# Kernel tuning notes

Hardware: AMD Instinct MI355X
Metric: run time of the kernel (lower is better)

The kernel has to match this reference:

```python
import jax, jax.numpy as jnp
import numpy as np


def setup_inputs() -> dict:
    key = jax.random.key(0)
    B, T, H, L = 64, 512, 768, 25
    ks = jax.random.split(key, 6)
    encoder_logits = jax.random.normal(ks[0], (B, T, H), dtype=jnp.float32)
    attention_mask = jnp.ones((B, T), dtype=jnp.int32)  # torchcrf requires mask[:,0]==1
    labels = jax.random.randint(ks[1], (B, T), 0, L, dtype=jnp.int32)
    W_em = jax.random.normal(ks[2], (H, L), dtype=jnp.float32) * 0.02
    b_em = jnp.zeros((L,), dtype=jnp.float32)
    # CRF.reset_parameters draws Uniform(-0.1, 0.1)
    trans = jax.random.uniform(ks[3], (L, L), minval=-0.1, maxval=0.1, dtype=jnp.float32)
    start_t = jax.random.uniform(ks[4], (L,), minval=-0.1, maxval=0.1, dtype=jnp.float32)
    end_t = jax.random.uniform(ks[5], (L,), minval=-0.1, maxval=0.1, dtype=jnp.float32)
    return {
        "encoder_logits": encoder_logits,
        "attention_mask": attention_mask,
        "labels": labels,
        "W_em": W_em,
        "b_em": b_em,
        "trans": trans,
        "start_t": start_t,
        "end_t": end_t,
    }


def _crf_llh(emissions, tags, mask, start_t, end_t, trans):
    # emissions: [B,T,L], tags: [B,T] int, mask: [B,T] {0,1}
    maskf = mask.astype(emissions.dtype)
    # ---- numerator: score of the gold path ----
    em_tag = jnp.take_along_axis(emissions, tags[..., None], axis=2)[..., 0]  # [B,T]
    num = start_t[tags[:, 0]] + em_tag[:, 0]
    tr = trans[tags[:, :-1], tags[:, 1:]]  # [B,T-1]
    num = num + jnp.sum((tr + em_tag[:, 1:]) * maskf[:, 1:], axis=1)
    last_idx = jnp.sum(mask, axis=1).astype(jnp.int32) - 1  # [B]
    last_tags = jnp.take_along_axis(tags, last_idx[:, None], axis=1)[:, 0]
    num = num + end_t[last_tags]
    # ---- denominator: log partition via forward algorithm (scan over time) ----
    alpha0 = start_t[None, :] + emissions[:, 0]  # [B,L]
    em_t = jnp.moveaxis(emissions[:, 1:], 1, 0)  # [T-1,B,L]
    m_t = jnp.moveaxis(maskf[:, 1:], 1, 0)       # [T-1,B]

    def step(alpha, xs):
        em, m = xs
        # broadcast [B,L,1] + [L,L] + [B,1,L] -> logsumexp over source tag
        nxt = jax.nn.logsumexp(alpha[:, :, None] + trans[None, :, :] + em[:, None, :], axis=1)
        return jnp.where(m[:, None] > 0, nxt, alpha), None

    alphaT, _ = jax.lax.scan(step, alpha0, (em_t, m_t))
    denom = jax.nn.logsumexp(alphaT + end_t[None, :], axis=1)  # [B]
    return num - denom


def reference(encoder_logits, attention_mask, labels, W_em, b_em, trans, start_t, end_t):
    # dropout layers are identity in eval mode
    emissions = jnp.einsum("bth,hl->btl", encoder_logits, W_em) + b_em
    llh = _crf_llh(emissions, labels, attention_mask, start_t, end_t, trans)
    # torchcrf reduction='mean' averages log-likelihood over batch; module returns -llh
    return -jnp.mean(llh)
```

## Files before the change

### kernel.cpp

```cpp
#include <hip/hip_runtime.h>
#include <hip/hip_bf16.h>

#define NB 64
#define NT 512
#define NH 768
#define NL 25
#define EST 28
#define SEGS 32
#define SEGLEN 16

typedef __attribute__((ext_vector_type(8))) short bf16x8;
typedef __attribute__((ext_vector_type(4))) float f32x4;
typedef __attribute__((ext_vector_type(16))) float f32x16;

__device__ __forceinline__ float readlane_f(float v, int k) {
  return __int_as_float(__builtin_amdgcn_readlane(__float_as_int(v), k));
}

__device__ __forceinline__ short f2bf(float x) {
  uint32_t u = __float_as_uint(x);
  uint32_t r = (u + 0x7fffu + ((u >> 16) & 1u)) >> 16;
  return (short)r;
}

__device__ __forceinline__ int cvt_pk_bf16(float lo, float hi) {
  int r;
  asm("v_cvt_pk_bf16_f32 %0, %1, %2" : "=v"(r) : "v"(lo), "v"(hi));
  return r;
}

__global__ __launch_bounds__(256) void emis_mfma_kernel(
    const float* __restrict__ X, const int* __restrict__ mask,
    const float* __restrict__ W, const float* __restrict__ bias,
    float* __restrict__ em) {
  __shared__ bf16x8 Bf[2][24][64];
  const int tid = threadIdx.x;

#pragma unroll
  for (int it = 0; it < 12; ++it) {
    int idx = tid + it * 256;
    int nt = idx / (24 * 64);
    int rem = idx - nt * (24 * 64);
    int ks = rem >> 6;
    int sl = rem & 63;
    int col = (sl & 15) + nt * 16;
    int kb = ks * 32 + (sl >> 4) * 8;
    bf16x8 f;
#pragma unroll
    for (int j = 0; j < 8; ++j) {
      float v = (col < NL) ? W[(kb + j) * NL + col] : 0.f;
      f[j] = f2bf(v);
    }
    Bf[nt][ks][sl] = f;
  }
  __syncthreads();

  const int wave = tid >> 6;
  const int lane = tid & 63;
  const int rowTile = blockIdx.x * 64 + wave * 16;
  const int row = rowTile + (lane & 15);
  const int koff = (lane >> 4) * 8;
  const float4* __restrict__ xr = (const float4*)(X + (size_t)row * NH + koff);

  f32x4 acc0 = {0.f, 0.f, 0.f, 0.f};
  f32x4 acc1 = {0.f, 0.f, 0.f, 0.f};
#pragma unroll 4
  for (int ks = 0; ks < 24; ++ks) {
    float4 xa = xr[ks * 8];
    float4 xb = xr[ks * 8 + 1];
    bf16x8 a;
    a[0] = f2bf(xa.x); a[1] = f2bf(xa.y); a[2] = f2bf(xa.z); a[3] = f2bf(xa.w);
    a[4] = f2bf(xb.x); a[5] = f2bf(xb.y); a[6] = f2bf(xb.z); a[7] = f2bf(xb.w);
    bf16x8 b0 = Bf[0][ks][lane];
    bf16x8 b1 = Bf[1][ks][lane];
    acc0 = __builtin_amdgcn_mfma_f32_16x16x32_bf16(a, b0, acc0, 0, 0, 0);
    acc1 = __builtin_amdgcn_mfma_f32_16x16x32_bf16(a, b1, acc1, 0, 0, 0);
  }

  const int cg = lane & 15;
  const int rbase = rowTile + (lane >> 4) * 4;
  float b0v = bias[cg];
  float b1v = (cg < 9) ? bias[16 + cg] : 0.f;
#pragma unroll
  for (int r = 0; r < 4; ++r) {
    int ro = rbase + r;
    float* er = em + (size_t)ro * EST;
    er[cg] = acc0[r] + b0v;
    if (cg < 9)       er[16 + cg] = acc1[r] + b1v;
    else if (cg == 9) er[25] = (float)mask[ro];
  }
}

__global__ __launch_bounds__(64) void crf_seg_kernel(
    const float* __restrict__ em, const float* __restrict__ trans,
    float* __restrict__ Dg, float* __restrict__ Dc) {
  const int b = blockIdx.x / SEGS;
  const int s = blockIdx.x % SEGS;
  const int lane = threadIdx.x;
  const int l = lane & 31;
  const int half = lane >> 5;
  const float* __restrict__ emb = em + (size_t)b * NT * EST;

  float Et0[8], Et1[8];
#pragma unroll
  for (int j = 0; j < 8; ++j) {
    int k0 = 8 * half + j;
    int k1 = 16 + 8 * half + j;
    Et0[j] = (l < NL) ? __expf(trans[k0 * NL + l]) : 0.f;
    Et1[j] = (l < NL && k1 < NL) ? __expf(trans[k1 * NL + l]) : 0.f;
  }

  f32x16 acc;
#pragma unroll
  for (int r = 0; r < 16; ++r) {
    int row = (r & 3) + 8 * (r >> 2) + 4 * half;
    acc[r] = (row == l && l < NL) ? 1.f : 0.f;
  }

  union Frag { int i[4]; bf16x8 v; };
  Frag B0, B1;
#pragma unroll
  for (int m = 0; m < 4; ++m) {
    int ka = 8 * half + 2 * m, kb = ka + 1;
    B0.i[m] = cvt_pk_bf16((ka == l && l < NL) ? 1.f : 0.f,
                          (kb == l && l < NL) ? 1.f : 0.f);
    int kc = 16 + 8 * half + 2 * m, kd = kc + 1;
    B1.i[m] = cvt_pk_bf16((kc == l && l < NL) ? 1.f : 0.f,
                          (kd == l && l < NL) ? 1.f : 0.f);
  }

  const int ts = 1 + s * SEGLEN;
  const int te = (ts + SEGLEN < NT) ? ts + SEGLEN : NT;
  const int c2 = (l < NL) ? l : NL;

  float c = 0.f, sc = 1.f, ei_ln2 = 0.f;

  float p0 = emb[ts * EST + c2];
  int i1 = ts + 1 < te ? ts + 1 : te - 1;
  int i2 = ts + 2 < te ? ts + 2 : te - 1;
  int i3 = ts + 3 < te ? ts + 3 : te - 1;
  float p1 = emb[i1 * EST + c2];
  float p2 = emb[i2 * EST + c2];
  float p3 = emb[i3 * EST + c2];

  for (int t = ts; t < te; ++t) {
    float emv = p0; p0 = p1; p1 = p2; p2 = p3;
    int tp = t + 4 < te ? t + 4 : te - 1;
    p3 = emb[tp * EST + c2];

    float mv = readlane_f(emv, 25);
    if (mv > 0.f) {
      float g = __expf(emv) * sc;
      c += ei_ln2;
      sc = 1.f; ei_ln2 = 0.f;

      Frag A0, A1;
#pragma unroll
      for (int m = 0; m < 4; ++m) {
        A0.i[m] = cvt_pk_bf16(Et0[2 * m] * g, Et0[2 * m + 1] * g);
        A1.i[m] = cvt_pk_bf16(Et1[2 * m] * g, Et1[2 * m + 1] * g);
      }
      f32x16 z;
#pragma unroll
      for (int r = 0; r < 16; ++r) z[r] = 0.f;
      z = __builtin_amdgcn_mfma_f32_32x32x16_bf16(A0.v, B0.v, z, 0, 0, 0);
      acc = __builtin_amdgcn_mfma_f32_32x32x16_bf16(A1.v, B1.v, z, 0, 0, 0);

      if ((t & 7) == 7) {
        float a0s = readlane_f(acc[0], 0);
        int eb = (__float_as_int(a0s) >> 23) & 255;
        int ei = (eb == 0) ? 0 : eb - 127;
        sc = __int_as_float((127 - ei) << 23);
        ei_ln2 = (float)ei * 0.6931471805599453f;
      }

      int u0 = cvt_pk_bf16(acc[0], acc[1]);
      int u1 = cvt_pk_bf16(acc[2], acc[3]);
      int w0 = cvt_pk_bf16(acc[4], acc[5]);
      int w1 = cvt_pk_bf16(acc[6], acc[7]);
      asm volatile("v_permlane32_swap_b32 %0, %1" : "+v"(u0), "+v"(w0));
      asm volatile("v_permlane32_swap_b32 %0, %1" : "+v"(u1), "+v"(w1));
      B0.i[0] = u0; B0.i[1] = u1; B0.i[2] = w0; B0.i[3] = w1;
      int v0 = cvt_pk_bf16(acc[8], acc[9]);
      int v1 = cvt_pk_bf16(acc[10], acc[11]);
      int x0 = cvt_pk_bf16(acc[12], acc[13]);
      int x1 = cvt_pk_bf16(acc[14], acc[15]);
      asm volatile("v_permlane32_swap_b32 %0, %1" : "+v"(v0), "+v"(x0));
      asm volatile("v_permlane32_swap_b32 %0, %1" : "+v"(v1), "+v"(x1));
      B1.i[0] = v0; B1.i[1] = v1; B1.i[2] = x0; B1.i[3] = x1;
    }
  }

  float* dst = Dg + (size_t)(b * SEGS + s) * 32 * 32;
#pragma unroll
  for (int r = 0; r < 16; ++r) {
    int row = (r & 3) + 8 * (r >> 2) + 4 * half;
    dst[row * 32 + l] = acc[r];
  }
  if (lane == 0) Dc[b * SEGS + s] = c;
}

__global__ __launch_bounds__(64) void crf_merge_kernel(
    const float* __restrict__ em, const int* __restrict__ labels,
    const int* __restrict__ mask, const float* __restrict__ trans,
    const float* __restrict__ start_t, const float* __restrict__ end_t,
    const float* __restrict__ Dg, const float* __restrict__ Dc,
    float* __restrict__ out) {
  const int b = blockIdx.x;
  const int lane = threadIdx.x;
  const float* __restrict__ emb = em + (size_t)b * NT * EST;
  const int* __restrict__ lb = labels + b * NT;
  const int* __restrict__ mk = mask + b * NT;

  float np = 0.f;
  int ms = 0;
#pragma unroll
  for (int i = 0; i < 8; ++i) {
    int t = lane + i * 64;
    int tag = lb[t];
    int m = mk[t];
    float emt = emb[t * EST + tag];
    ms += m;
    if (t == 0) {
      np += start_t[tag] + emt;
    } else {
      int tagp = lb[t - 1];
      np += (trans[tagp * NL + tag] + emt) * (float)m;
    }
  }
#pragma unroll
  for (int off = 32; off > 0; off >>= 1) {
    np += __shfl_down(np, off, 64);
    ms += __shfl_down(ms, off, 64);
  }
  float num = 0.f;
  if (lane == 0) num = np + end_t[lb[ms - 1]];

  const int l = lane & 31;
  float a = (lane < NL) ? __expf(start_t[lane] + emb[lane]) : 0.f;
  float c = 0.f;
  for (int s = 0; s < SEGS; ++s) {
    const float* Drow = Dg + ((size_t)(b * SEGS + s) * 32 + l) * 32;
    float a0 = 0.f, a1 = 0.f, a2 = 0.f, a3 = 0.f;
#pragma unroll
    for (int i = 0; i < NL; i += 4) {
      a0 = fmaf(Drow[i], readlane_f(a, i), a0);
      if (i + 1 < NL) a1 = fmaf(Drow[i + 1], readlane_f(a, i + 1), a1);
      if (i + 2 < NL) a2 = fmaf(Drow[i + 2], readlane_f(a, i + 2), a2);
      if (i + 3 < NL) a3 = fmaf(Drow[i + 3], readlane_f(a, i + 3), a3);
    }
    float an = (a0 + a1) + (a2 + a3);
    c += Dc[b * SEGS + s];
    float s0 = readlane_f(an, 0);
    int eb = (__float_as_int(s0) >> 23) & 255;
    int ei = (eb == 0) ? 0 : eb - 127;
    a = an * __int_as_float((127 - ei) << 23);
    c += (float)ei * 0.6931471805599453f;
  }

  float v = (lane < NL) ? a * __expf(end_t[lane]) : 0.f;
#pragma unroll
  for (int off = 32; off > 0; off >>= 1) v += __shfl_down(v, off, 64);
  if (lane == 0) {
    float denom = c + __logf(v);
    atomicAdd(out, (denom - num) * (1.0f / (float)NB));
  }
}

__global__ __launch_bounds__(64) void crf_kernel(
    const float* __restrict__ em, const int* __restrict__ labels,
    const int* __restrict__ mask, const float* __restrict__ trans,
    const float* __restrict__ start_t, const float* __restrict__ end_t,
    float* __restrict__ out) {
  const int b = blockIdx.x;
  const int lane = threadIdx.x;
  const int l = lane < NL ? lane : NL - 1;
  const float* __restrict__ emb = em + (size_t)b * NT * EST;
  const int* __restrict__ lb = labels + b * NT;
  const int* __restrict__ mk = mask + b * NT;

  float np = 0.f;
  int ms = 0;
#pragma unroll
  for (int i = 0; i < 8; ++i) {
    int t = lane + i * 64;
    int tag = lb[t];
    int m = mk[t];
    float emt = emb[t * EST + tag];
    ms += m;
    if (t == 0) np += start_t[tag] + emt;
    else {
      int tagp = lb[t - 1];
      np += (trans[tagp * NL + tag] + emt) * (float)m;
    }
  }
#pragma unroll
  for (int off = 32; off > 0; off >>= 1) {
    np += __shfl_down(np, off, 64);
    ms += __shfl_down(ms, off, 64);
  }
  float num = 0.f;
  if (lane == 0) num = np + end_t[lb[ms - 1]];

  float Ecol[NL];
#pragma unroll
  for (int k = 0; k < NL; ++k) Ecol[k] = __expf(trans[k * NL + l]);

  float A = __expf(start_t[l] + emb[l]);
  float c = 0.f, sc = 1.f, ei_ln2 = 0.f;
  const int j = lane < NL ? lane : NL;

  float p1 = emb[1 * EST + j];
  float p2 = emb[2 * EST + j];
  float p3 = emb[3 * EST + j];
  float p4 = emb[4 * EST + j];

  for (int t = 1; t < NT; ++t) {
    float emv = p1;
    p1 = p2; p2 = p3; p3 = p4;
    int tp = t + 4; tp = tp < NT ? tp : NT - 1;
    p4 = emb[tp * EST + j];
    float e_em = __expf(emv);
    float Pv0 = 0.f, Pv1 = 0.f, Pv2 = 0.f, Pv3 = 0.f;
#pragma unroll
    for (int k = 0; k < NL; k += 4) {
      Pv0 = fmaf(readlane_f(A, k), Ecol[k], Pv0);
      if (k + 1 < NL) Pv1 = fmaf(readlane_f(A, k + 1), Ecol[k + 1], Pv1);
      if (k + 2 < NL) Pv2 = fmaf(readlane_f(A, k + 2), Ecol[k + 2], Pv2);
      if (k + 3 < NL) Pv3 = fmaf(readlane_f(A, k + 3), Ecol[k + 3], Pv3);
    }
    float g = ((Pv0 + Pv1) + (Pv2 + Pv3)) * e_em;
    float mfv = readlane_f(emv, 25);
    float An = (mfv > 0.f) ? g : A;
    A = An * sc;
    c += ei_ln2;
    float a0 = readlane_f(A, 0);
    int eb = (__float_as_int(a0) >> 23) & 255;
    int ei = (eb == 0) ? 0 : (eb - 127);
    sc = __int_as_float((127 - ei) << 23);
    ei_ln2 = (float)ei * 0.6931471805599453f;
  }

  float v = (lane < NL) ? A * __expf(end_t[l]) : 0.f;
#pragma unroll
  for (int off = 32; off > 0; off >>= 1) v += __shfl_down(v, off, 64);
  if (lane == 0) {
    float denom = c + __logf(v);
    atomicAdd(out, (denom - num) * (1.0f / (float)NB));
  }
}

extern "C" void kernel_launch(void* const* d_in, const int* in_sizes, int n_in,
                              void* d_out, int out_size, void* d_ws, size_t ws_size,
                              hipStream_t stream) {
  const float* X       = (const float*)d_in[0];
  const int*   mask    = (const int*)d_in[1];
  const int*   labels  = (const int*)d_in[2];
  const float* W       = (const float*)d_in[3];
  const float* bias    = (const float*)d_in[4];
  const float* trans   = (const float*)d_in[5];
  const float* start_t = (const float*)d_in[6];
  const float* end_t   = (const float*)d_in[7];
  float* out = (float*)d_out;

  float* em = (float*)d_ws;
  float* Dg = (float*)((char*)d_ws + (4u << 20));
  float* Dc = (float*)((char*)d_ws + (4u << 20) + (8u << 20));

  hipMemsetAsync(out, 0, sizeof(float), stream);
  emis_mfma_kernel<<<512, 256, 0, stream>>>(X, mask, W, bias, em);
  if (ws_size >= (13u << 20)) {
    crf_seg_kernel<<<NB * SEGS, 64, 0, stream>>>(em, trans, Dg, Dc);
    crf_merge_kernel<<<NB, 64, 0, stream>>>(em, labels, mask, trans, start_t,
                                            end_t, Dg, Dc, out);
  } else {
    crf_kernel<<<NB, 64, 0, stream>>>(em, labels, mask, trans, start_t, end_t, out);
  }
}
```

Measured before the change: 198.7 us.

## Pre-pack W into bf16 MFMA fragments and compute emissions without LDS

Adds a small kernel that converts W once per call into bf16 MFMA B-fragment layout in workspace. The emission GEMM becomes a one-wave-per-16-row kernel that reads X and the packed W straight from global memory, with no LDS staging or per-block W conversion. The aim is to remove the repeated per-block conversion of W and the LDS traffic, and to raise parallelism to 2048 small blocks. The cost is an extra kernel launch and redundant global/L2 reads of the packed W by every wave. The workspace layout shifts and the fast path now requires a larger workspace.

```diff
diff --git a/kernel.cpp b/kernel.cpp
--- a/kernel.cpp
+++ b/kernel.cpp
@@ -13,6 +13,8 @@
 typedef __attribute__((ext_vector_type(4))) float f32x4;
 typedef __attribute__((ext_vector_type(16))) float f32x16;
 
+union Frag { int i[4]; bf16x8 v; };
+
 __device__ __forceinline__ float readlane_f(float v, int k) {
   return __int_as_float(__builtin_amdgcn_readlane(__float_as_int(v), k));
 }
@@ -27,6 +29,68 @@
   int r;
   asm("v_cvt_pk_bf16_f32 %0, %1, %2" : "=v"(r) : "v"(lo), "v"(hi));
   return r;
+}
+
+__global__ __launch_bounds__(256) void pack_w_kernel(
+    const float* __restrict__ W, bf16x8* __restrict__ Wp) {
+  int idx = blockIdx.x * 256 + threadIdx.x;
+  int nt = idx / (24 * 64);
+  int rem = idx - nt * (24 * 64);
+  int ks = rem >> 6;
+  int sl = rem & 63;
+  int col = (sl & 15) + nt * 16;
+  int kb = ks * 32 + (sl >> 4) * 8;
+  Frag f;
+#pragma unroll
+  for (int m = 0; m < 4; ++m) {
+    float lo = (col < NL) ? W[(kb + 2 * m) * NL + col] : 0.f;
+    float hi = (col < NL) ? W[(kb + 2 * m + 1) * NL + col] : 0.f;
+    f.i[m] = cvt_pk_bf16(lo, hi);
+  }
+  Wp[idx] = f.v;
+}
+
+__global__ __launch_bounds__(64) void emis_nolds_kernel(
+    const float* __restrict__ X, const int* __restrict__ mask,
+    const bf16x8* __restrict__ Wp, const float* __restrict__ bias,
+    float* __restrict__ em) {
+  const int lane = threadIdx.x;
+  const int rowTile = blockIdx.x * 16;
+  const int row = rowTile + (lane & 15);
+  const int koff = (lane >> 4) * 8;
+  const float4* __restrict__ xr = (const float4*)(X + (size_t)row * NH + koff);
+  const bf16x8* __restrict__ w0 = Wp + lane;
+  const bf16x8* __restrict__ w1 = Wp + 24 * 64 + lane;
+
+  f32x4 acc0 = {0.f, 0.f, 0.f, 0.f};
+  f32x4 acc1 = {0.f, 0.f, 0.f, 0.f};
+#pragma unroll 4
+  for (int ks = 0; ks < 24; ++ks) {
+    float4 xa = xr[ks * 8];
+    float4 xb = xr[ks * 8 + 1];
+    bf16x8 b0 = w0[ks * 64];
+    bf16x8 b1 = w1[ks * 64];
+    Frag a;
+    a.i[0] = cvt_pk_bf16(xa.x, xa.y);
+    a.i[1] = cvt_pk_bf16(xa.z, xa.w);
+    a.i[2] = cvt_pk_bf16(xb.x, xb.y);
+    a.i[3] = cvt_pk_bf16(xb.z, xb.w);
+    acc0 = __builtin_amdgcn_mfma_f32_16x16x32_bf16(a.v, b0, acc0, 0, 0, 0);
+    acc1 = __builtin_amdgcn_mfma_f32_16x16x32_bf16(a.v, b1, acc1, 0, 0, 0);
+  }
+
+  const int cg = lane & 15;
+  const int rbase = rowTile + (lane >> 4) * 4;
+  float b0v = bias[cg];
+  float b1v = (cg < 9) ? bias[16 + cg] : 0.f;
+#pragma unroll
+  for (int r = 0; r < 4; ++r) {
+    int ro = rbase + r;
+    float* er = em + (size_t)ro * EST;
+    er[cg] = acc0[r] + b0v;
+    if (cg < 9)       er[16 + cg] = acc1[r] + b1v;
+    else if (cg == 9) er[25] = (float)mask[ro];
+  }
 }
 
 __global__ __launch_bounds__(256) void emis_mfma_kernel(
@@ -117,7 +181,6 @@
     acc[r] = (row == l && l < NL) ? 1.f : 0.f;
   }
 
-  union Frag { int i[4]; bf16x8 v; };
   Frag B0, B1;
 #pragma unroll
   for (int m = 0; m < 4; ++m) {
@@ -363,17 +426,21 @@
   const float* end_t   = (const float*)d_in[7];
   float* out = (float*)d_out;
 
-  float* em = (float*)d_ws;
-  float* Dg = (float*)((char*)d_ws + (4u << 20));
-  float* Dc = (float*)((char*)d_ws + (4u << 20) + (8u << 20));
+  char* ws = (char*)d_ws;
+  float*  em = (float*)ws;
+  float*  Dg = (float*)(ws + (4u << 20));
+  float*  Dc = (float*)(ws + (12u << 20));
+  bf16x8* Wp = (bf16x8*)(ws + (12u << 20) + 65536);
 
   hipMemsetAsync(out, 0, sizeof(float), stream);
-  emis_mfma_kernel<<<512, 256, 0, stream>>>(X, mask, W, bias, em);
-  if (ws_size >= (13u << 20)) {
+  if (ws_size >= (14u << 20)) {
+    pack_w_kernel<<<12, 256, 0, stream>>>(W, Wp);
+    emis_nolds_kernel<<<2048, 64, 0, stream>>>(X, mask, Wp, bias, em);
     crf_seg_kernel<<<NB * SEGS, 64, 0, stream>>>(em, trans, Dg, Dc);
     crf_merge_kernel<<<NB, 64, 0, stream>>>(em, labels, mask, trans, start_t,
                                             end_t, Dg, Dc, out);
   } else {
+    emis_mfma_kernel<<<512, 256, 0, stream>>>(X, mask, W, bias, em);
     crf_kernel<<<NB, 64, 0, stream>>>(em, labels, mask, trans, start_t, end_t, out);
   }
 }
```

After: 198.2 us. Within noise of the previous version (-0.2%).
